# Kernel tuning notes

Measured on AMD Instinct MI355X. Metric: run time of the kernel, lower is better.

Reference implementation:

```python
import jax, jax.numpy as jnp
import numpy as np

N, NC, E = 100000, 50000, 1600000   # source points, centers, edges
D, P, H, O = 64, 3, 128, 128        # feat dim, pos dim, hidden, out


def setup_inputs() -> dict:
    key = jax.random.key(0)
    ks = jax.random.split(key, 10)
    x = jax.random.normal(ks[0], (N, D), jnp.float32)
    x_c = jax.random.normal(ks[1], (NC, O), jnp.float32)  # only shape is used
    pos = jax.random.normal(ks[2], (N, P), jnp.float32)
    pos_c = jax.random.normal(ks[3], (NC, P), jnp.float32)
    src = jax.random.randint(ks[4], (E,), 0, N)
    dst = jax.random.randint(ks[5], (E,), 0, NC)
    W1 = jax.random.normal(ks[6], (D + P, H), jnp.float32) / jnp.sqrt(D + P)
    b1 = jnp.zeros((H,), jnp.float32)
    W2 = jax.random.normal(ks[7], (H, O), jnp.float32) / jnp.sqrt(H)
    b2 = jnp.zeros((O,), jnp.float32)
    return dict(x=x, x_c=x_c, pos=pos, pos_c=pos_c, src=src, dst=dst,
                W1=W1, b1=b1, W2=W2, b2=b2)


def reference(x, x_c, pos, pos_c, src, dst, W1, b1, W2, b2):
    # gather per-edge features: [E, D+P]
    feats = jnp.concatenate([x[src], pos[src] - pos_c[dst]], axis=1)
    # MLP on edges
    h = jax.nn.relu(feats @ W1 + b1) @ W2 + b2  # [E, O]
    # scatter-max aggregation onto centers
    agg = jax.ops.segment_max(h, dst, num_segments=x_c.shape[0])  # [NC, O]
    # match torch_scatter convention: empty segments -> 0 (not -inf)
    return jnp.where(jnp.isneginf(agg), 0.0, agg)
```

## Files before the change

kernel.cpp:

```cpp
#include <hip/hip_runtime.h>
#include <hip/hip_bf16.h>

#define NPTS   100000
#define NCENT  50000
#define NEDGE  1600000
#define DF     64
#define DP     3
#define DH     128
#define DOUT   128
#define TILE   128
#define LDA    104
#define LDH    136
#define LDE    132
#define NCPAD  50176

typedef __attribute__((ext_vector_type(8))) short short8;
typedef __attribute__((ext_vector_type(4))) float f32x4;

__device__ __forceinline__ unsigned short f2bf(float f) {
  union { __hip_bfloat16 h; unsigned short u; } v;
  v.h = __float2bfloat16(f);
  return v.u;
}

__device__ __forceinline__ unsigned encodeKey(float f) {
  unsigned u = __float_as_uint(f);
  return u ^ ((unsigned)((int)u >> 31) | 0x80000000u);
}

__device__ __forceinline__ float decodeKey(unsigned k) {
  if (k == 0u) return 0.0f;
  unsigned u = (k & 0x80000000u) ? (k ^ 0x80000000u) : ~k;
  return __uint_as_float(u);
}

__global__ void k_prep(const float* __restrict__ x, const float* __restrict__ W1,
                       const float* __restrict__ W2, const int* __restrict__ dst,
                       unsigned short* __restrict__ xbf, unsigned short* __restrict__ W1f,
                       unsigned short* __restrict__ W2f, int* __restrict__ cnt,
                       unsigned short* __restrict__ rank, unsigned* __restrict__ outU) {
  const int b = blockIdx.x;
  const int t = threadIdx.x;
  if (b < 6250) {
    int i = b * 256 + t;
    rank[i] = (unsigned short)atomicAdd(&cnt[dst[i]], 1);
  } else if (b < 12500) {
    int i = (b - 6250) * 256 + t;
    reinterpret_cast<uint4*>(outU)[i] = make_uint4(0u, 0u, 0u, 0u);
  } else if (b < 15625) {
    int i = (b - 12500) * 256 + t;
    const float4* xr = reinterpret_cast<const float4*>(x);
    float4 v0 = xr[2 * i], v1 = xr[2 * i + 1];
    short8 w;
    w[0] = (short)f2bf(v0.x); w[1] = (short)f2bf(v0.y);
    w[2] = (short)f2bf(v0.z); w[3] = (short)f2bf(v0.w);
    w[4] = (short)f2bf(v1.x); w[5] = (short)f2bf(v1.y);
    w[6] = (short)f2bf(v1.z); w[7] = (short)f2bf(v1.w);
    reinterpret_cast<short8*>(xbf)[i] = w;
  } else if (b < 15631) {
    int tid = (b - 15625) * 256 + t;
    int lane = tid & 63, g = tid >> 6;
    int nt = g / 3, ks = g % 3;
    int n = nt * 16 + (lane & 15);
    int k0 = ks * 32 + (lane >> 4) * 8;
    short8 v;
    for (int j = 0; j < 8; ++j) {
      int k = k0 + j;
      float f = (k < DF + DP) ? W1[k * DH + n] : 0.0f;
      v[j] = (short)f2bf(f);
    }
    *reinterpret_cast<short8*>(W1f + (size_t)tid * 8) = v;
  } else {
    int tid = (b - 15631) * 256 + t;
    int lane = tid & 63, g = tid >> 6;
    int nt = g >> 2, ks = g & 3;
    int n = nt * 16 + (lane & 15);
    int k0 = ks * 32 + (lane >> 4) * 8;
    short8 v;
    for (int j = 0; j < 8; ++j) {
      int k = k0 + j;
      v[j] = (short)f2bf(W2[k * DH + n]);
    }
    *reinterpret_cast<short8*>(W2f + (size_t)tid * 8) = v;
  }
}


__global__ void k_s1(const int* __restrict__ cnt, int* __restrict__ bsum) {
  __shared__ int sh[256];
  int t = threadIdx.x;
  sh[t] = cnt[blockIdx.x * 256 + t];
  __syncthreads();
  for (int off = 128; off > 0; off >>= 1) {
    if (t < off) sh[t] += sh[t + off];
    __syncthreads();
  }
  if (t == 0) bsum[blockIdx.x] = sh[0];
}

__global__ void k_s23(int* __restrict__ cnt, const int* __restrict__ bsum) {
  __shared__ int sh[256];
  __shared__ int pre;
  const int t = threadIdx.x;
  const int i = blockIdx.x * 256 + t;
  sh[t] = (t < blockIdx.x && t < 196) ? bsum[t] : 0;
  __syncthreads();
  for (int off = 128; off > 0; off >>= 1) {
    if (t < off) sh[t] += sh[t + off];
    __syncthreads();
  }
  if (t == 0) pre = sh[0];
  __syncthreads();
  int v = cnt[i];
  sh[t] = v;
  __syncthreads();
  for (int off = 1; off < 256; off <<= 1) {
    int u = (t >= off) ? sh[t - off] : 0;
    __syncthreads();
    sh[t] += u;
    __syncthreads();
  }
  cnt[i] = sh[t] - v + pre;
}

__global__ void k_place(const int* __restrict__ src, const int* __restrict__ dst,
                        const int* __restrict__ base, const unsigned short* __restrict__ rank,
                        unsigned long long* __restrict__ sdS) {
  int i = blockIdx.x * 256 + threadIdx.x;
  int d = dst[i];
  int p = base[d] + (int)rank[i];
  sdS[p] = ((unsigned long long)(unsigned)d << 32) | (unsigned)src[i];
}

__global__ void k_decode(unsigned* __restrict__ out) {
  int i = blockIdx.x * blockDim.x + threadIdx.x;
  uint4 v = reinterpret_cast<uint4*>(out)[i];
  float4 f;
  f.x = decodeKey(v.x);
  f.y = decodeKey(v.y);
  f.z = decodeKey(v.z);
  f.w = decodeKey(v.w);
  reinterpret_cast<float4*>(out)[i] = f;
}

__global__ void __launch_bounds__(256, 4)
k_mlp(const unsigned short* __restrict__ xbf, const float* __restrict__ pos,
      const float* __restrict__ pos_c, const unsigned long long* __restrict__ sdS,
      const float* __restrict__ b1, const float* __restrict__ b2,
      const unsigned short* __restrict__ W1f, const unsigned short* __restrict__ W2f,
      unsigned* __restrict__ outU) {
  __shared__ __align__(16) unsigned short buf[TILE * LDH];
  __shared__ int dstLoc[TILE];

  const int t = threadIdx.x;
  const int e0 = blockIdx.x * TILE;

  {
    const int e = t >> 1, p = t & 1;
    const unsigned long long rec = sdS[e0 + e];
    const int s = (int)(rec & 0xffffffffu);
    const short8* xr = reinterpret_cast<const short8*>(xbf + (size_t)s * DF);
    for (int i = 0; i < 4; ++i)
      *reinterpret_cast<short8*>(&buf[e * LDA + p * 32 + i * 8]) = xr[p * 4 + i];
    short8 z = {0, 0, 0, 0, 0, 0, 0, 0};
    *reinterpret_cast<short8*>(&buf[e * LDA + 72 + p * 16]) = z;
    *reinterpret_cast<short8*>(&buf[e * LDA + 72 + p * 16 + 8]) = z;
  }
  if (t < TILE) {
    const unsigned long long rec = sdS[e0 + t];
    const int s = (int)(rec & 0xffffffffu);
    const int c = (int)(rec >> 32);
    dstLoc[t] = c;
    float dx = pos[(size_t)s * 3 + 0] - pos_c[(size_t)c * 3 + 0];
    float dy = pos[(size_t)s * 3 + 1] - pos_c[(size_t)c * 3 + 1];
    float dz = pos[(size_t)s * 3 + 2] - pos_c[(size_t)c * 3 + 2];
    short8 w = {0, 0, 0, 0, 0, 0, 0, 0};
    w[0] = (short)f2bf(dx); w[1] = (short)f2bf(dy); w[2] = (short)f2bf(dz);
    *reinterpret_cast<short8*>(&buf[t * LDA + 64]) = w;
  }
  __syncthreads();

  const int lane = t & 63;
  const int w = t >> 6;
  const int l16 = lane & 15;
  const int quad = lane >> 4;

  short8 a1[2][3];
  for (int mi = 0; mi < 2; ++mi) {
    int row = (2 * w + mi) * 16 + l16;
    for (int ks = 0; ks < 3; ++ks)
      a1[mi][ks] = *reinterpret_cast<const short8*>(&buf[row * LDA + ks * 32 + quad * 8]);
  }
  __syncthreads();

  for (int nt = 0; nt < 8; ++nt) {
    short8 b[3];
    for (int ks = 0; ks < 3; ++ks)
      b[ks] = *reinterpret_cast<const short8*>(W1f + ((size_t)(nt * 3 + ks) * 64 + lane) * 8);
    f32x4 acc0 = {0.f, 0.f, 0.f, 0.f}, acc1 = {0.f, 0.f, 0.f, 0.f};
    for (int ks = 0; ks < 3; ++ks) {
      acc0 = __builtin_amdgcn_mfma_f32_16x16x32_bf16(a1[0][ks], b[ks], acc0, 0, 0, 0);
      acc1 = __builtin_amdgcn_mfma_f32_16x16x32_bf16(a1[1][ks], b[ks], acc1, 0, 0, 0);
    }
    int n = nt * 16 + l16;
    float bias = b1[n];
    for (int r = 0; r < 4; ++r) {
      float v0 = acc0[r] + bias; v0 = v0 > 0.f ? v0 : 0.f;
      buf[((2 * w) * 16 + quad * 4 + r) * LDH + n] = f2bf(v0);
      float v1 = acc1[r] + bias; v1 = v1 > 0.f ? v1 : 0.f;
      buf[((2 * w + 1) * 16 + quad * 4 + r) * LDH + n] = f2bf(v1);
    }
  }
  __syncthreads();

  short8 a2[2][4];
  for (int mi = 0; mi < 2; ++mi) {
    int row = (2 * w + mi) * 16 + l16;
    for (int ks = 0; ks < 4; ++ks)
      a2[mi][ks] = *reinterpret_cast<const short8*>(&buf[row * LDH + ks * 32 + quad * 8]);
  }
  __syncthreads();

  float* Sf = reinterpret_cast<float*>(buf);
  const int col = t & 63;
  const int chunk = t >> 6;

  unsigned mask32;
  {
    int pred = 0;
    if (lane > 0 && lane < 32)
      pred = (dstLoc[chunk * 32 + lane] != dstLoc[chunk * 32 + lane - 1]) ? 1 : 0;
    mask32 = (unsigned)(__ballot(pred) & 0xffffffffull);
  }

  for (int half = 0; half < 2; ++half) {
    for (int ntl = 0; ntl < 4; ++ntl) {
      const int nt = half * 4 + ntl;
      short8 b[4];
      for (int ks = 0; ks < 4; ++ks)
        b[ks] = *reinterpret_cast<const short8*>(W2f + ((size_t)(nt * 4 + ks) * 64 + lane) * 8);
      f32x4 acc0 = {0.f, 0.f, 0.f, 0.f}, acc1 = {0.f, 0.f, 0.f, 0.f};
      for (int ks = 0; ks < 4; ++ks) {
        acc0 = __builtin_amdgcn_mfma_f32_16x16x32_bf16(a2[0][ks], b[ks], acc0, 0, 0, 0);
        acc1 = __builtin_amdgcn_mfma_f32_16x16x32_bf16(a2[1][ks], b[ks], acc1, 0, 0, 0);
      }
      const int nl = ntl * 16 + l16;
      const float bias = b2[half * 64 + nl];
      for (int r = 0; r < 4; ++r) { acc0[r] += bias; acc1[r] += bias; }
      *reinterpret_cast<f32x4*>(&Sf[nl * LDE + (2 * w) * 16 + quad * 4]) = acc0;
      *reinterpret_cast<f32x4*>(&Sf[nl * LDE + (2 * w + 1) * 16 + quad * 4]) = acc1;
    }
    __syncthreads();
    float running = -3.402823466e38f;
    const float* row = &Sf[col * LDE + chunk * 32];
    for (int g = 0; g < 8; ++g) {
      f32x4 v = *reinterpret_cast<const f32x4*>(row + 4 * g);
      unsigned bits = (mask32 >> (4 * g)) & 0xFu;
      if (bits == 0u) {
        running = fmaxf(running, fmaxf(fmaxf(v[0], v[1]), fmaxf(v[2], v[3])));
      } else {
        for (int j = 0; j < 4; ++j) {
          if ((bits >> j) & 1u) {
            int dprev = dstLoc[chunk * 32 + 4 * g + j - 1];
            atomicMax(&outU[(size_t)dprev * DOUT + half * 64 + col], encodeKey(running));
            running = -3.402823466e38f;
          }
          running = fmaxf(running, v[j]);
        }
      }
    }
    int dlast = dstLoc[chunk * 32 + 31];
    atomicMax(&outU[(size_t)dlast * DOUT + half * 64 + col], encodeKey(running));
    __syncthreads();
  }
}

extern "C" void kernel_launch(void* const* d_in, const int* in_sizes, int n_in,
                              void* d_out, int out_size, void* d_ws, size_t ws_size,
                              hipStream_t stream) {
  const float* x     = (const float*)d_in[0];
  const float* pos   = (const float*)d_in[2];
  const float* pos_c = (const float*)d_in[3];
  const int*   src   = (const int*)d_in[4];
  const int*   dst   = (const int*)d_in[5];
  const float* W1    = (const float*)d_in[6];
  const float* b1    = (const float*)d_in[7];
  const float* W2    = (const float*)d_in[8];
  const float* b2    = (const float*)d_in[9];
  unsigned* outU = (unsigned*)d_out;

  char* base = (char*)d_ws;
  unsigned short* W1f = (unsigned short*)base;
  unsigned short* W2f = (unsigned short*)(base + 24576);
  int* bsum  = (int*)(base + 57344);
  int* cnt   = (int*)(base + 65536);
  unsigned short* rank = (unsigned short*)(base + 266240);
  unsigned long long* sdS = (unsigned long long*)(base + 3466240);
  unsigned short* xbf = (unsigned short*)(base + 16266240);

  hipMemsetAsync(cnt, 0, NCPAD * sizeof(int), stream);
  k_prep<<<15639, 256, 0, stream>>>(x, W1, W2, dst, xbf, W1f, W2f, cnt, rank, outU);
  k_s1<<<NCPAD / 256, 256, 0, stream>>>(cnt, bsum);
  k_s23<<<NCPAD / 256, 256, 0, stream>>>(cnt, bsum);
  k_place<<<NEDGE / 256, 256, 0, stream>>>(src, dst, cnt, rank, sdS);
  k_mlp<<<NEDGE / TILE, 256, 0, stream>>>(xbf, pos, pos_c, sdS,
                                          b1, b2, W1f, W2f, outU);
  k_decode<<<(NCENT * DOUT / 4) / 256, 256, 0, stream>>>(outU);
}
```

Measured before the change: 364.3 us.

## Fuse all stages into one persistent cooperative kernel with grid-wide syncs

Merges the prep, count, two scan stages, placement, edge MLP and decode kernels into a single cooperative kernel. A persistent grid (up to 1024 blocks) runs each stage with grid-stride loops, separated by grid.sync. This removes six launches and the memset, but adds five grid barriers and limits the MLP phase to the persistent block count instead of 12500 independent blocks. The cooperative launch also requires every block to be resident at once.

```diff
diff --git a/kernel.cpp b/kernel.cpp
--- a/kernel.cpp
+++ b/kernel.cpp
@@ -1,5 +1,8 @@
 #include <hip/hip_runtime.h>
 #include <hip/hip_bf16.h>
+#include <hip/hip_cooperative_groups.h>
+
+namespace cg = cooperative_groups;
 
 #define NPTS   100000
 #define NCENT  50000
@@ -9,6 +12,7 @@
 #define DH     128
 #define DOUT   128
 #define TILE   128
+#define NTILES (NEDGE / TILE)
 #define LDA    104
 #define LDH    136
 #define LDE    132
@@ -34,21 +38,30 @@
   return __uint_as_float(u);
 }
 
-__global__ void k_prep(const float* __restrict__ x, const float* __restrict__ W1,
-                       const float* __restrict__ W2, const int* __restrict__ dst,
-                       unsigned short* __restrict__ xbf, unsigned short* __restrict__ W1f,
-                       unsigned short* __restrict__ W2f, int* __restrict__ cnt,
-                       unsigned short* __restrict__ rank, unsigned* __restrict__ outU) {
+__global__ void __launch_bounds__(256, 4)
+k_all(const float* __restrict__ x, const float* __restrict__ pos,
+      const float* __restrict__ pos_c, const int* __restrict__ src,
+      const int* __restrict__ dstE, const float* __restrict__ W1,
+      const float* __restrict__ b1, const float* __restrict__ W2,
+      const float* __restrict__ b2, unsigned* __restrict__ outU,
+      unsigned short* __restrict__ xbf, unsigned short* __restrict__ W1f,
+      unsigned short* __restrict__ W2f, int* __restrict__ cnt,
+      unsigned short* __restrict__ rankA, int* __restrict__ bsum,
+      unsigned long long* __restrict__ sdS) {
+  cg::grid_group grid = cg::this_grid();
+  __shared__ __align__(16) unsigned short buf[TILE * LDH];
+  __shared__ int dstLoc[TILE];
+  __shared__ int pre_s;
+
+  const int t = threadIdx.x;
   const int b = blockIdx.x;
-  const int t = threadIdx.x;
-  if (b < 6250) {
-    int i = b * 256 + t;
-    rank[i] = (unsigned short)atomicAdd(&cnt[dst[i]], 1);
-  } else if (b < 12500) {
-    int i = (b - 6250) * 256 + t;
+  const int tid = b * 256 + t;
+  const int gsz = gridDim.x * 256;
+
+  if (tid < NCPAD) cnt[tid] = 0;
+  for (int i = tid; i < NCENT * DOUT / 4; i += gsz)
     reinterpret_cast<uint4*>(outU)[i] = make_uint4(0u, 0u, 0u, 0u);
-  } else if (b < 15625) {
-    int i = (b - 12500) * 256 + t;
+  for (int i = tid; i < NPTS * DF / 8; i += gsz) {
     const float4* xr = reinterpret_cast<const float4*>(x);
     float4 v0 = xr[2 * i], v1 = xr[2 * i + 1];
     short8 w;
@@ -57,8 +70,8 @@
     w[4] = (short)f2bf(v1.x); w[5] = (short)f2bf(v1.y);
     w[6] = (short)f2bf(v1.z); w[7] = (short)f2bf(v1.w);
     reinterpret_cast<short8*>(xbf)[i] = w;
-  } else if (b < 15631) {
-    int tid = (b - 15625) * 256 + t;
+  }
+  if (tid < 1536) {
     int lane = tid & 63, g = tid >> 6;
     int nt = g / 3, ks = g % 3;
     int n = nt * 16 + (lane & 15);
@@ -70,9 +83,9 @@
       v[j] = (short)f2bf(f);
     }
     *reinterpret_cast<short8*>(W1f + (size_t)tid * 8) = v;
-  } else {
-    int tid = (b - 15631) * 256 + t;
-    int lane = tid & 63, g = tid >> 6;
+  } else if (tid >= 2048 && tid < 4096) {
+    int t2 = tid - 2048;
+    int lane = t2 & 63, g = t2 >> 6;
     int nt = g >> 2, ks = g & 3;
     int n = nt * 16 + (lane & 15);
     int k0 = ks * 32 + (lane >> 4) * 8;
@@ -81,197 +94,187 @@
       int k = k0 + j;
       v[j] = (short)f2bf(W2[k * DH + n]);
     }
-    *reinterpret_cast<short8*>(W2f + (size_t)tid * 8) = v;
-  }
-}
-
-
-__global__ void k_s1(const int* __restrict__ cnt, int* __restrict__ bsum) {
-  __shared__ int sh[256];
-  int t = threadIdx.x;
-  sh[t] = cnt[blockIdx.x * 256 + t];
-  __syncthreads();
-  for (int off = 128; off > 0; off >>= 1) {
-    if (t < off) sh[t] += sh[t + off];
-    __syncthreads();
-  }
-  if (t == 0) bsum[blockIdx.x] = sh[0];
-}
-
-__global__ void k_s23(int* __restrict__ cnt, const int* __restrict__ bsum) {
-  __shared__ int sh[256];
-  __shared__ int pre;
-  const int t = threadIdx.x;
-  const int i = blockIdx.x * 256 + t;
-  sh[t] = (t < blockIdx.x && t < 196) ? bsum[t] : 0;
-  __syncthreads();
-  for (int off = 128; off > 0; off >>= 1) {
-    if (t < off) sh[t] += sh[t + off];
-    __syncthreads();
-  }
-  if (t == 0) pre = sh[0];
-  __syncthreads();
-  int v = cnt[i];
-  sh[t] = v;
-  __syncthreads();
-  for (int off = 1; off < 256; off <<= 1) {
-    int u = (t >= off) ? sh[t - off] : 0;
-    __syncthreads();
-    sh[t] += u;
-    __syncthreads();
-  }
-  cnt[i] = sh[t] - v + pre;
-}
-
-__global__ void k_place(const int* __restrict__ src, const int* __restrict__ dst,
-                        const int* __restrict__ base, const unsigned short* __restrict__ rank,
-                        unsigned long long* __restrict__ sdS) {
-  int i = blockIdx.x * 256 + threadIdx.x;
-  int d = dst[i];
-  int p = base[d] + (int)rank[i];
-  sdS[p] = ((unsigned long long)(unsigned)d << 32) | (unsigned)src[i];
-}
-
-__global__ void k_decode(unsigned* __restrict__ out) {
-  int i = blockIdx.x * blockDim.x + threadIdx.x;
-  uint4 v = reinterpret_cast<uint4*>(out)[i];
-  float4 f;
-  f.x = decodeKey(v.x);
-  f.y = decodeKey(v.y);
-  f.z = decodeKey(v.z);
-  f.w = decodeKey(v.w);
-  reinterpret_cast<float4*>(out)[i] = f;
-}
-
-__global__ void __launch_bounds__(256, 4)
-k_mlp(const unsigned short* __restrict__ xbf, const float* __restrict__ pos,
-      const float* __restrict__ pos_c, const unsigned long long* __restrict__ sdS,
-      const float* __restrict__ b1, const float* __restrict__ b2,
-      const unsigned short* __restrict__ W1f, const unsigned short* __restrict__ W2f,
-      unsigned* __restrict__ outU) {
-  __shared__ __align__(16) unsigned short buf[TILE * LDH];
-  __shared__ int dstLoc[TILE];
-
-  const int t = threadIdx.x;
-  const int e0 = blockIdx.x * TILE;
-
-  {
-    const int e = t >> 1, p = t & 1;
-    const unsigned long long rec = sdS[e0 + e];
-    const int s = (int)(rec & 0xffffffffu);
-    const short8* xr = reinterpret_cast<const short8*>(xbf + (size_t)s * DF);
-    for (int i = 0; i < 4; ++i)
-      *reinterpret_cast<short8*>(&buf[e * LDA + p * 32 + i * 8]) = xr[p * 4 + i];
-    short8 z = {0, 0, 0, 0, 0, 0, 0, 0};
-    *reinterpret_cast<short8*>(&buf[e * LDA + 72 + p * 16]) = z;
-    *reinterpret_cast<short8*>(&buf[e * LDA + 72 + p * 16 + 8]) = z;
-  }
-  if (t < TILE) {
-    const unsigned long long rec = sdS[e0 + t];
-    const int s = (int)(rec & 0xffffffffu);
-    const int c = (int)(rec >> 32);
-    dstLoc[t] = c;
-    float dx = pos[(size_t)s * 3 + 0] - pos_c[(size_t)c * 3 + 0];
-    float dy = pos[(size_t)s * 3 + 1] - pos_c[(size_t)c * 3 + 1];
-    float dz = pos[(size_t)s * 3 + 2] - pos_c[(size_t)c * 3 + 2];
-    short8 w = {0, 0, 0, 0, 0, 0, 0, 0};
-    w[0] = (short)f2bf(dx); w[1] = (short)f2bf(dy); w[2] = (short)f2bf(dz);
-    *reinterpret_cast<short8*>(&buf[t * LDA + 64]) = w;
-  }
-  __syncthreads();
+    *reinterpret_cast<short8*>(W2f + (size_t)t2 * 8) = v;
+  }
+  grid.sync();
+
+  for (int i = tid; i < NEDGE; i += gsz)
+    rankA[i] = (unsigned short)atomicAdd(&cnt[dstE[i]], 1);
+  grid.sync();
+
+  int* shi = reinterpret_cast<int*>(buf);
+  if (b < NCPAD / 256) {
+    shi[t] = cnt[b * 256 + t];
+    __syncthreads();
+    for (int off = 128; off > 0; off >>= 1) {
+      if (t < off) shi[t] += shi[t + off];
+      __syncthreads();
+    }
+    if (t == 0) bsum[b] = shi[0];
+  }
+  grid.sync();
+
+  if (b < NCPAD / 256) {
+    shi[t] = (t < b) ? bsum[t] : 0;
+    __syncthreads();
+    for (int off = 128; off > 0; off >>= 1) {
+      if (t < off) shi[t] += shi[t + off];
+      __syncthreads();
+    }
+    if (t == 0) pre_s = shi[0];
+    __syncthreads();
+    int v = cnt[b * 256 + t];
+    shi[t] = v;
+    __syncthreads();
+    for (int off = 1; off < 256; off <<= 1) {
+      int u = (t >= off) ? shi[t - off] : 0;
+      __syncthreads();
+      shi[t] += u;
+      __syncthreads();
+    }
+    cnt[b * 256 + t] = shi[t] - v + pre_s;
+  }
+  grid.sync();
+
+  for (int i = tid; i < NEDGE; i += gsz) {
+    int d = dstE[i];
+    int p = cnt[d] + (int)rankA[i];
+    sdS[p] = ((unsigned long long)(unsigned)d << 32) | (unsigned)src[i];
+  }
+  grid.sync();
 
   const int lane = t & 63;
   const int w = t >> 6;
   const int l16 = lane & 15;
   const int quad = lane >> 4;
 
-  short8 a1[2][3];
-  for (int mi = 0; mi < 2; ++mi) {
-    int row = (2 * w + mi) * 16 + l16;
-    for (int ks = 0; ks < 3; ++ks)
-      a1[mi][ks] = *reinterpret_cast<const short8*>(&buf[row * LDA + ks * 32 + quad * 8]);
-  }
-  __syncthreads();
-
-  for (int nt = 0; nt < 8; ++nt) {
-    short8 b[3];
-    for (int ks = 0; ks < 3; ++ks)
-      b[ks] = *reinterpret_cast<const short8*>(W1f + ((size_t)(nt * 3 + ks) * 64 + lane) * 8);
-    f32x4 acc0 = {0.f, 0.f, 0.f, 0.f}, acc1 = {0.f, 0.f, 0.f, 0.f};
-    for (int ks = 0; ks < 3; ++ks) {
-      acc0 = __builtin_amdgcn_mfma_f32_16x16x32_bf16(a1[0][ks], b[ks], acc0, 0, 0, 0);
-      acc1 = __builtin_amdgcn_mfma_f32_16x16x32_bf16(a1[1][ks], b[ks], acc1, 0, 0, 0);
-    }
-    int n = nt * 16 + l16;
-    float bias = b1[n];
-    for (int r = 0; r < 4; ++r) {
-      float v0 = acc0[r] + bias; v0 = v0 > 0.f ? v0 : 0.f;
-      buf[((2 * w) * 16 + quad * 4 + r) * LDH + n] = f2bf(v0);
-      float v1 = acc1[r] + bias; v1 = v1 > 0.f ? v1 : 0.f;
-      buf[((2 * w + 1) * 16 + quad * 4 + r) * LDH + n] = f2bf(v1);
-    }
-  }
-  __syncthreads();
-
-  short8 a2[2][4];
-  for (int mi = 0; mi < 2; ++mi) {
-    int row = (2 * w + mi) * 16 + l16;
-    for (int ks = 0; ks < 4; ++ks)
-      a2[mi][ks] = *reinterpret_cast<const short8*>(&buf[row * LDH + ks * 32 + quad * 8]);
-  }
-  __syncthreads();
-
-  float* Sf = reinterpret_cast<float*>(buf);
-  const int col = t & 63;
-  const int chunk = t >> 6;
-
-  unsigned mask32;
-  {
-    int pred = 0;
-    if (lane > 0 && lane < 32)
-      pred = (dstLoc[chunk * 32 + lane] != dstLoc[chunk * 32 + lane - 1]) ? 1 : 0;
-    mask32 = (unsigned)(__ballot(pred) & 0xffffffffull);
-  }
-
-  for (int half = 0; half < 2; ++half) {
-    for (int ntl = 0; ntl < 4; ++ntl) {
-      const int nt = half * 4 + ntl;
-      short8 b[4];
+  for (int tile = b; tile < NTILES; tile += gridDim.x) {
+    const int e0 = tile * TILE;
+
+    {
+      const int e = t >> 1, p = t & 1;
+      const unsigned long long rec = sdS[e0 + e];
+      const int s = (int)(rec & 0xffffffffu);
+      const short8* xr = reinterpret_cast<const short8*>(xbf + (size_t)s * DF);
+      for (int i = 0; i < 4; ++i)
+        *reinterpret_cast<short8*>(&buf[e * LDA + p * 32 + i * 8]) = xr[p * 4 + i];
+      short8 z = {0, 0, 0, 0, 0, 0, 0, 0};
+      *reinterpret_cast<short8*>(&buf[e * LDA + 72 + p * 16]) = z;
+      *reinterpret_cast<short8*>(&buf[e * LDA + 72 + p * 16 + 8]) = z;
+    }
+    if (t < TILE) {
+      const unsigned long long rec = sdS[e0 + t];
+      const int s = (int)(rec & 0xffffffffu);
+      const int c = (int)(rec >> 32);
+      dstLoc[t] = c;
+      float dx = pos[(size_t)s * 3 + 0] - pos_c[(size_t)c * 3 + 0];
+      float dy = pos[(size_t)s * 3 + 1] - pos_c[(size_t)c * 3 + 1];
+      float dz = pos[(size_t)s * 3 + 2] - pos_c[(size_t)c * 3 + 2];
+      short8 wv = {0, 0, 0, 0, 0, 0, 0, 0};
+      wv[0] = (short)f2bf(dx); wv[1] = (short)f2bf(dy); wv[2] = (short)f2bf(dz);
+      *reinterpret_cast<short8*>(&buf[t * LDA + 64]) = wv;
+    }
+    __syncthreads();
+
+    short8 a1[2][3];
+    for (int mi = 0; mi < 2; ++mi) {
+      int row = (2 * w + mi) * 16 + l16;
+      for (int ks = 0; ks < 3; ++ks)
+        a1[mi][ks] = *reinterpret_cast<const short8*>(&buf[row * LDA + ks * 32 + quad * 8]);
+    }
+    __syncthreads();
+
+    for (int nt = 0; nt < 8; ++nt) {
+      short8 bb[3];
+      for (int ks = 0; ks < 3; ++ks)
+        bb[ks] = *reinterpret_cast<const short8*>(W1f + ((size_t)(nt * 3 + ks) * 64 + lane) * 8);
+      f32x4 acc0 = {0.f, 0.f, 0.f, 0.f}, acc1 = {0.f, 0.f, 0.f, 0.f};
+      for (int ks = 0; ks < 3; ++ks) {
+        acc0 = __builtin_amdgcn_mfma_f32_16x16x32_bf16(a1[0][ks], bb[ks], acc0, 0, 0, 0);
+        acc1 = __builtin_amdgcn_mfma_f32_16x16x32_bf16(a1[1][ks], bb[ks], acc1, 0, 0, 0);
+      }
+      int n = nt * 16 + l16;
+      float bias = b1[n];
+      for (int r = 0; r < 4; ++r) {
+        float v0 = acc0[r] + bias; v0 = v0 > 0.f ? v0 : 0.f;
+        buf[((2 * w) * 16 + quad * 4 + r) * LDH + n] = f2bf(v0);
+        float v1 = acc1[r] + bias; v1 = v1 > 0.f ? v1 : 0.f;
+        buf[((2 * w + 1) * 16 + quad * 4 + r) * LDH + n] = f2bf(v1);
+      }
+    }
+    __syncthreads();
+
+    short8 a2[2][4];
+    for (int mi = 0; mi < 2; ++mi) {
+      int row = (2 * w + mi) * 16 + l16;
       for (int ks = 0; ks < 4; ++ks)
-        b[ks] = *reinterpret_cast<const short8*>(W2f + ((size_t)(nt * 4 + ks) * 64 + lane) * 8);
-      f32x4 acc0 = {0.f, 0.f, 0.f, 0.f}, acc1 = {0.f, 0.f, 0.f, 0.f};
-      for (int ks = 0; ks < 4; ++ks) {
-        acc0 = __builtin_amdgcn_mfma_f32_16x16x32_bf16(a2[0][ks], b[ks], acc0, 0, 0, 0);
-        acc1 = __builtin_amdgcn_mfma_f32_16x16x32_bf16(a2[1][ks], b[ks], acc1, 0, 0, 0);
+        a2[mi][ks] = *reinterpret_cast<const short8*>(&buf[row * LDH + ks * 32 + quad * 8]);
+    }
+    __syncthreads();
+
+    float* Sf = reinterpret_cast<float*>(buf);
+    const int col = t & 63;
+    const int chunk = t >> 6;
+
+    unsigned mask32;
+    {
+      int pred = 0;
+      if (lane > 0 && lane < 32)
+        pred = (dstLoc[chunk * 32 + lane] != dstLoc[chunk * 32 + lane - 1]) ? 1 : 0;
+      mask32 = (unsigned)(__ballot(pred) & 0xffffffffull);
+    }
+
+    for (int half = 0; half < 2; ++half) {
+      for (int ntl = 0; ntl < 4; ++ntl) {
+        const int nt = half * 4 + ntl;
+        short8 bb[4];
+        for (int ks = 0; ks < 4; ++ks)
+          bb[ks] = *reinterpret_cast<const short8*>(W2f + ((size_t)(nt * 4 + ks) * 64 + lane) * 8);
+        f32x4 acc0 = {0.f, 0.f, 0.f, 0.f}, acc1 = {0.f, 0.f, 0.f, 0.f};
+        for (int ks = 0; ks < 4; ++ks) {
+          acc0 = __builtin_amdgcn_mfma_f32_16x16x32_bf16(a2[0][ks], bb[ks], acc0, 0, 0, 0);
+          acc1 = __builtin_amdgcn_mfma_f32_16x16x32_bf16(a2[1][ks], bb[ks], acc1, 0, 0, 0);
+        }
+        const int nl = ntl * 16 + l16;
+        const float bias = b2[half * 64 + nl];
+        for (int r = 0; r < 4; ++r) { acc0[r] += bias; acc1[r] += bias; }
+        *reinterpret_cast<f32x4*>(&Sf[nl * LDE + (2 * w) * 16 + quad * 4]) = acc0;
+        *reinterpret_cast<f32x4*>(&Sf[nl * LDE + (2 * w + 1) * 16 + quad * 4]) = acc1;
       }
-      const int nl = ntl * 16 + l16;
-      const float bias = b2[half * 64 + nl];
-      for (int r = 0; r < 4; ++r) { acc0[r] += bias; acc1[r] += bias; }
-      *reinterpret_cast<f32x4*>(&Sf[nl * LDE + (2 * w) * 16 + quad * 4]) = acc0;
-      *reinterpret_cast<f32x4*>(&Sf[nl * LDE + (2 * w + 1) * 16 + quad * 4]) = acc1;
-    }
-    __syncthreads();
-    float running = -3.402823466e38f;
-    const float* row = &Sf[col * LDE + chunk * 32];
-    for (int g = 0; g < 8; ++g) {
-      f32x4 v = *reinterpret_cast<const f32x4*>(row + 4 * g);
-      unsigned bits = (mask32 >> (4 * g)) & 0xFu;
-      if (bits == 0u) {
-        running = fmaxf(running, fmaxf(fmaxf(v[0], v[1]), fmaxf(v[2], v[3])));
-      } else {
-        for (int j = 0; j < 4; ++j) {
-          if ((bits >> j) & 1u) {
-            int dprev = dstLoc[chunk * 32 + 4 * g + j - 1];
-            atomicMax(&outU[(size_t)dprev * DOUT + half * 64 + col], encodeKey(running));
-            running = -3.402823466e38f;
+      __syncthreads();
+      float running = -3.402823466e38f;
+      const float* row = &Sf[col * LDE + chunk * 32];
+      for (int g = 0; g < 8; ++g) {
+        f32x4 v = *reinterpret_cast<const f32x4*>(row + 4 * g);
+        unsigned bits = (mask32 >> (4 * g)) & 0xFu;
+        if (bits == 0u) {
+          running = fmaxf(running, fmaxf(fmaxf(v[0], v[1]), fmaxf(v[2], v[3])));
+        } else {
+          for (int j = 0; j < 4; ++j) {
+            if ((bits >> j) & 1u) {
+              int dprev = dstLoc[chunk * 32 + 4 * g + j - 1];
+              atomicMax(&outU[(size_t)dprev * DOUT + half * 64 + col], encodeKey(running));
+              running = -3.402823466e38f;
+            }
+            running = fmaxf(running, v[j]);
           }
-          running = fmaxf(running, v[j]);
         }
       }
-    }
-    int dlast = dstLoc[chunk * 32 + 31];
-    atomicMax(&outU[(size_t)dlast * DOUT + half * 64 + col], encodeKey(running));
-    __syncthreads();
+      int dlast = dstLoc[chunk * 32 + 31];
+      atomicMax(&outU[(size_t)dlast * DOUT + half * 64 + col], encodeKey(running));
+      __syncthreads();
+    }
+  }
+  grid.sync();
+
+  for (int i = tid; i < NCENT * DOUT / 4; i += gsz) {
+    uint4 v = reinterpret_cast<uint4*>(outU)[i];
+    float4 f;
+    f.x = decodeKey(v.x);
+    f.y = decodeKey(v.y);
+    f.z = decodeKey(v.z);
+    f.w = decodeKey(v.w);
+    reinterpret_cast<float4*>(outU)[i] = f;
   }
 }
 
@@ -298,12 +301,19 @@
   unsigned long long* sdS = (unsigned long long*)(base + 3466240);
   unsigned short* xbf = (unsigned short*)(base + 16266240);
 
-  hipMemsetAsync(cnt, 0, NCPAD * sizeof(int), stream);
-  k_prep<<<15639, 256, 0, stream>>>(x, W1, W2, dst, xbf, W1f, W2f, cnt, rank, outU);
-  k_s1<<<NCPAD / 256, 256, 0, stream>>>(cnt, bsum);
-  k_s23<<<NCPAD / 256, 256, 0, stream>>>(cnt, bsum);
-  k_place<<<NEDGE / 256, 256, 0, stream>>>(src, dst, cnt, rank, sdS);
-  k_mlp<<<NEDGE / TILE, 256, 0, stream>>>(xbf, pos, pos_c, sdS,
-                                          b1, b2, W1f, W2f, outU);
-  k_decode<<<(NCENT * DOUT / 4) / 256, 256, 0, stream>>>(outU);
-}
+  int perCU = 0;
+  if (hipOccupancyMaxActiveBlocksPerMultiprocessor(&perCU, k_all, 256, 0) != hipSuccess
+      || perCU < 1)
+    perCU = 1;
+  int nblk = perCU * 256;
+  if (nblk > 1024) nblk = 1024;
+  if (nblk < 256) nblk = 256;
+
+  void* args[] = {
+    (void*)&x, (void*)&pos, (void*)&pos_c, (void*)&src, (void*)&dst,
+    (void*)&W1, (void*)&b1, (void*)&W2, (void*)&b2, (void*)&outU,
+    (void*)&xbf, (void*)&W1f, (void*)&W2f, (void*)&cnt, (void*)&rank,
+    (void*)&bsum, (void*)&sdS
+  };
+  hipLaunchCooperativeKernel(k_all, dim3(nblk), dim3(256), args, 0, stream);
+}
```

Measured after the change: 831.9 us. +128.3%, slower.
